# Optimization experiments

Measured on AMD Instinct MI355X. Metric: run time of the kernel, lower is better.

Reference implementation:

```python
import jax, jax.numpy as jnp
import numpy as np

TEMP = 0.07
EPS = 1e-6

B = 8192
D1 = 129  # d+1 ambient Lorentz coords


def setup_inputs() -> dict:
    key = jax.random.key(0)
    k1, k2 = jax.random.split(key)
    z1 = jax.random.normal(k1, (B, D1), dtype=jnp.float32)
    z2 = jax.random.normal(k2, (B, D1), dtype=jnp.float32)
    return {"z1": z1, "z2": z2}


def _loss(z1, z2):
    # Minkowski (Lorentz) inner product via a single GEMM:
    # <x,y>_L = -x0*y0 + sum_i xi*yi  ->  x @ (metric * y)^T
    metric = jnp.concatenate([-jnp.ones((1,), z1.dtype), jnp.ones((D1 - 1,), z1.dtype)])
    inner = jnp.einsum('bd,kd->bk', z1, z2 * metric)  # (B, B)
    # Lorentz distance with curvature c=1: acosh(clamp(-<x,y>_L, 1+eps))
    dist = jnp.arccosh(jnp.clip(-inner, 1.0 + EPS, None))
    sims = -dist / TEMP
    # symmetric InfoNCE: labels are the diagonal
    logp_t2i = jax.nn.log_softmax(sims, axis=-1)      # text -> image
    logp_i2t = jax.nn.log_softmax(sims.T, axis=-1)    # image -> text
    diag = jnp.arange(sims.shape[0])
    loss_t2i = -jnp.mean(logp_t2i[diag, diag])
    loss_i2t = -jnp.mean(logp_i2t[diag, diag])
    return (loss_t2i + loss_i2t) / 2.0


def reference(z1, z2):
    return _loss(z1, z2)
```

## Files before the change

### kernel.cpp

```cpp
#include <hip/hip_runtime.h>
#include <math.h>


#define BDIM   8192
#define K_IN   129
#define K_PAD  160
#define BK     32
#define NKT    (K_PAD / BK)
#define CTILES 8

typedef __bf16  bf16x8 __attribute__((ext_vector_type(8)));
typedef float   f32x4  __attribute__((ext_vector_type(4)));

#define OFF_A    0u
#define OFF_B    (BDIM * K_PAD * 2u)
#define OFF_RS   (2u * BDIM * K_PAD * 2u)
#define OFF_CP   (OFF_RS + BDIM * 4u)
#define OFF_DG   (OFF_CP + 4u * BDIM * 4u)

__device__ __forceinline__ float fast_sqrt(float x) {
#if __has_builtin(__builtin_amdgcn_sqrtf)
    return __builtin_amdgcn_sqrtf(x);
#else
    return sqrtf(x);
#endif
}
__device__ __forceinline__ float fast_log2(float x) {
#if __has_builtin(__builtin_amdgcn_logf)
    return __builtin_amdgcn_logf(x);
#else
    return __log2f(x);
#endif
}
__device__ __forceinline__ float fast_exp2(float x) {
#if __has_builtin(__builtin_amdgcn_exp2f)
    return __builtin_amdgcn_exp2f(x);
#else
    extern "C" __device__ float __ocml_native_exp2_f32(float);
    return __ocml_native_exp2_f32(x);
#endif
}

__device__ __forceinline__ unsigned short f2bf_rne(float f) {
    unsigned int u = __float_as_uint(f);
    u += 0x7FFFu + ((u >> 16) & 1u);
    return (unsigned short)(u >> 16);
}

__global__ __launch_bounds__(256) void convert_kernel(
    const float* __restrict__ z1, const float* __restrict__ z2,
    unsigned short* __restrict__ A, unsigned short* __restrict__ B,
    float* __restrict__ rs_cp)
{
    int idx = blockIdx.x * 256 + threadIdx.x;
    if (idx < 5 * BDIM) rs_cp[idx] = 0.f;
    if (idx >= BDIM * K_PAD) return;
    int r = idx / K_PAD;
    int c = idx - r * K_PAD;
    float va = 0.f, vb = 0.f;
    if (c < K_IN) {
        va = z1[r * K_IN + c];
        vb = z2[r * K_IN + c];
        if (c == 0) va = -va;
    }
    A[idx] = f2bf_rne(va);
    B[idx] = f2bf_rne(vb);
}


#define STAGE(bufidx, cb)                                                     \
    {                                                                         \
        const char* _gp = (const char*)(B + (size_t)(cb) * K_PAD)             \
                          + wave * 5120 + lane * 16;                          \
        unsigned short* _lp = &Bs[bufidx][wave * 2560];                       \
        _Pragma("unroll")                                                     \
        for (int _i = 0; _i < 5; ++_i)                                        \
            __builtin_amdgcn_global_load_lds(                                 \
                (const __attribute__((address_space(1))) void*)               \
                    (_gp + _i * 1024),                                        \
                (__attribute__((address_space(3))) void*)(_lp + _i * 512),    \
                16, 0, 0);                                                    \
    }

#define COMPUTE(bufidx, cb)                                                   \
    {                                                                         \
        const int colBase = (cb);                                             \
        const unsigned short* _Bt = &Bs[bufidx][0];                           \
        f32x4 acc[2][4] = {};                                                 \
        _Pragma("unroll")                                                     \
        for (int kt = 0; kt < NKT; ++kt) {                                    \
            bf16x8 bfr[4];                                                    \
            _Pragma("unroll")                                                 \
            for (int j = 0; j < 4; ++j)                                       \
                bfr[j] = *(const bf16x8*)                                     \
                    &_Bt[(l16 + j * 16) * K_PAD + quad * 8 + kt * BK];        \
            _Pragma("unroll")                                                 \
            for (int i = 0; i < 2; ++i)                                       \
                _Pragma("unroll")                                             \
                for (int j = 0; j < 4; ++j)                                   \
                    acc[i][j] = __builtin_amdgcn_mfma_f32_16x16x32_bf16(      \
                        Ah[i][kt], bfr[j], acc[i][j], 0, 0, 0);               \
        }                                                                     \
        const bool diagTile = (colBase == (rowBase & ~63));                   \
        const int  dj       = (rowBase >> 4) & 2;                             \
        float colp[4] = {0.f, 0.f, 0.f, 0.f};                                 \
        _Pragma("unroll")                                                     \
        for (int i = 0; i < 2; ++i) {                                         \
            _Pragma("unroll")                                                 \
            for (int j = 0; j < 4; ++j) {                                     \
                _Pragma("unroll")                                             \
                for (int reg = 0; reg < 4; ++reg) {                           \
                    float inner = acc[i][j][reg];                             \
                    float x = fmaxf(-inner, 1.000001f);                       \
                    float s = fast_sqrt(__builtin_fmaf(x, x, -1.0f));         \
                    float l2u = fast_log2(x + s);                             \
                    float e = fast_exp2(-14.285714285714286f * l2u);          \
                    rowp[i][reg] += e;                                        \
                    colp[j]      += e;                                        \
                    if (diagTile && (j - i) == dj && (quad * 4 + reg) == l16){\
                        int R = rowBase + i * 16 + quad * 4 + reg;            \
                        diag[R] = -9.902102579427789f * l2u;                  \
                    }                                                         \
                }                                                             \
            }                                                                 \
        }                                                                     \
        _Pragma("unroll")                                                     \
        for (int j = 0; j < 4; ++j) {                                         \
            float v = colp[j];                                                \
            v += __shfl_xor(v, 16);                                           \
            v += __shfl_xor(v, 32);                                           \
            if (quad == 0)                                                    \
                atomicAdd(&colRep[colBase + j * 16 + l16], v);                \
        }                                                                     \
    }

__global__ __launch_bounds__(256, 3) void gemm_epilogue_kernel(
    const unsigned short* __restrict__ A, const unsigned short* __restrict__ B,
    float* __restrict__ row_sum, float* __restrict__ col_part,
    float* __restrict__ diag)
{
    const int t    = threadIdx.x;
    const int lane = t & 63;
    const int wave = t >> 6;
    const int quad = lane >> 4;
    const int l16  = lane & 15;

    const int strip = blockIdx.x & 63;
    const int chunk = blockIdx.x >> 6;
    const int rowBase  = strip * 128 + wave * 32;
    const int colChunk = chunk * 512;

    const unsigned short* Abase = A + (rowBase + l16) * K_PAD + quad * 8;
    float* colRep = col_part + (strip & 3) * BDIM;

    __shared__ __align__(16) unsigned short Bs[2][64 * K_PAD];

    bf16x8 Ah[2][NKT];
    #pragma unroll
    for (int i = 0; i < 2; ++i)
        #pragma unroll
        for (int kt = 0; kt < NKT; ++kt)
            Ah[i][kt] = *(const bf16x8*)(Abase + i * 16 * K_PAD + kt * BK);

    float rowp[2][4] = {};

    STAGE(0, colChunk);
    __syncthreads();

    #pragma unroll 1
    for (int ct = 0; ct < CTILES; ++ct) {
        if (ct + 1 < CTILES)
            STAGE((ct + 1) & 1, colChunk + (ct + 1) * 64);
        COMPUTE(ct & 1, colChunk + ct * 64);
        __syncthreads();
    }

    #pragma unroll
    for (int i = 0; i < 2; ++i) {
        #pragma unroll
        for (int reg = 0; reg < 4; ++reg) {
            float v = rowp[i][reg];
            v += __shfl_xor(v, 1);
            v += __shfl_xor(v, 2);
            v += __shfl_xor(v, 4);
            v += __shfl_xor(v, 8);
            if (l16 == 0)
                atomicAdd(&row_sum[rowBase + i * 16 + quad * 4 + reg], v);
        }
    }
}

__global__ __launch_bounds__(1024) void finalize_kernel(
    const float* __restrict__ rs, const float* __restrict__ cp,
    const float* __restrict__ dg, float* __restrict__ out)
{
    __shared__ float part[16];
    int t = threadIdx.x;
    float a = 0.f;
    const float LN2_HALF = 0.34657359027997264f;
    for (int b = t; b < BDIM; b += 1024) {
        float cs = cp[b] + cp[b + BDIM] + cp[b + 2 * BDIM] + cp[b + 3 * BDIM];
        a += LN2_HALF * (fast_log2(rs[b]) + fast_log2(cs)) - dg[b];
    }
    #pragma unroll
    for (int m = 1; m < 64; m <<= 1) a += __shfl_xor(a, m);
    if ((t & 63) == 0) part[t >> 6] = a;
    __syncthreads();
    if (t < 16) {
        float v = part[t];
        #pragma unroll
        for (int m = 1; m < 16; m <<= 1) v += __shfl_xor(v, m);
        if (t == 0) out[0] = v * (1.0f / (float)BDIM);
    }
}

extern "C" void kernel_launch(void* const* d_in, const int* in_sizes, int n_in,
                              void* d_out, int out_size, void* d_ws, size_t ws_size,
                              hipStream_t stream)
{
    const float* z1 = (const float*)d_in[0];
    const float* z2 = (const float*)d_in[1];
    float* out = (float*)d_out;

    char* ws = (char*)d_ws;
    unsigned short* A  = (unsigned short*)(ws + OFF_A);
    unsigned short* B  = (unsigned short*)(ws + OFF_B);
    float* row_sum     = (float*)(ws + OFF_RS);
    float* col_part    = (float*)(ws + OFF_CP);
    float* diag        = (float*)(ws + OFF_DG);

    convert_kernel<<<(BDIM * K_PAD + 255) / 256, 256, 0, stream>>>(
        z1, z2, A, B, row_sum );

    gemm_epilogue_kernel<<<1024, 256, 0, stream>>>(
        A, B, row_sum, col_part, diag);

    finalize_kernel<<<1, 1024, 0, stream>>>(row_sum, col_part, diag, out);
}
```

Before: 108.8 us.

## Accumulate column sums in LDS and vectorize bf16 conversion stores

Column partial sums are now accumulated per block in a shared-memory array and flushed once to global memory with interleaved replica layout, instead of issuing global atomics every column tile. The convert kernel now writes 8 bf16 values per thread with vector stores, and the finalize kernel reads the four column replicas with one vector load. This reduces global atomic traffic and launch/thread count for conversion, at the cost of LDS atomics and a small extra shared buffer that may affect occupancy.

```diff
diff --git a/kernel.cpp b/kernel.cpp
--- a/kernel.cpp
+++ b/kernel.cpp
@@ -6,11 +6,12 @@
 #define K_IN   129
 #define K_PAD  160
 #define BK     32
-#define NKT    (K_PAD / BK)
+#define NKT    5
 #define CTILES 8
 
 typedef __bf16  bf16x8 __attribute__((ext_vector_type(8)));
 typedef float   f32x4  __attribute__((ext_vector_type(4)));
+typedef unsigned short u16x8 __attribute__((ext_vector_type(8)));
 
 #define OFF_A    0u
 #define OFF_B    (BDIM * K_PAD * 2u)
@@ -52,19 +53,26 @@
     unsigned short* __restrict__ A, unsigned short* __restrict__ B,
     float* __restrict__ rs_cp)
 {
-    int idx = blockIdx.x * 256 + threadIdx.x;
-    if (idx < 5 * BDIM) rs_cp[idx] = 0.f;
-    if (idx >= BDIM * K_PAD) return;
-    int r = idx / K_PAD;
-    int c = idx - r * K_PAD;
-    float va = 0.f, vb = 0.f;
-    if (c < K_IN) {
-        va = z1[r * K_IN + c];
-        vb = z2[r * K_IN + c];
-        if (c == 0) va = -va;
-    }
-    A[idx] = f2bf_rne(va);
-    B[idx] = f2bf_rne(vb);
+    int v = blockIdx.x * 256 + threadIdx.x;
+    if (v < 5 * BDIM) rs_cp[v] = 0.f;
+    if (v >= BDIM * (K_PAD / 8)) return;
+    int r  = v / (K_PAD / 8);
+    int c8 = (v - r * (K_PAD / 8)) * 8;
+    u16x8 a, b;
+    #pragma unroll
+    for (int i = 0; i < 8; ++i) {
+        int c = c8 + i;
+        float va = 0.f, vb = 0.f;
+        if (c < K_IN) {
+            va = z1[r * K_IN + c];
+            vb = z2[r * K_IN + c];
+            if (c == 0) va = -va;
+        }
+        a[i] = f2bf_rne(va);
+        b[i] = f2bf_rne(vb);
+    }
+    *(u16x8*)(A + r * K_PAD + c8) = a;
+    *(u16x8*)(B + r * K_PAD + c8) = b;
 }
 
 
@@ -130,7 +138,7 @@
             v += __shfl_xor(v, 16);                                           \
             v += __shfl_xor(v, 32);                                           \
             if (quad == 0)                                                    \
-                atomicAdd(&colRep[colBase + j * 16 + l16], v);                \
+                atomicAdd(&colAcc[(colBase - colChunk) + j * 16 + l16], v);   \
         }                                                                     \
     }
 
@@ -151,9 +159,11 @@
     const int colChunk = chunk * 512;
 
     const unsigned short* Abase = A + (rowBase + l16) * K_PAD + quad * 8;
-    float* colRep = col_part + (strip & 3) * BDIM;
 
     __shared__ __align__(16) unsigned short Bs[2][64 * K_PAD];
+    __shared__ float colAcc[512];
+
+    for (int c = t; c < 512; c += 256) colAcc[c] = 0.f;
 
     bf16x8 Ah[2][NKT];
     #pragma unroll
@@ -188,6 +198,9 @@
                 atomicAdd(&row_sum[rowBase + i * 16 + quad * 4 + reg], v);
         }
     }
+    const int rep = strip & 3;
+    for (int c = t; c < 512; c += 256)
+        atomicAdd(&col_part[(colChunk + c) * 4 + rep], colAcc[c]);
 }
 
 __global__ __launch_bounds__(1024) void finalize_kernel(
@@ -199,7 +212,8 @@
     float a = 0.f;
     const float LN2_HALF = 0.34657359027997264f;
     for (int b = t; b < BDIM; b += 1024) {
-        float cs = cp[b] + cp[b + BDIM] + cp[b + 2 * BDIM] + cp[b + 3 * BDIM];
+        f32x4 cv = *(const f32x4*)&cp[b * 4];
+        float cs = cv[0] + cv[1] + cv[2] + cv[3];
         a += LN2_HALF * (fast_log2(rs[b]) + fast_log2(cs)) - dg[b];
     }
     #pragma unroll
@@ -229,7 +243,7 @@
     float* col_part    = (float*)(ws + OFF_CP);
     float* diag        = (float*)(ws + OFF_DG);
 
-    convert_kernel<<<(BDIM * K_PAD + 255) / 256, 256, 0, stream>>>(
+    convert_kernel<<<(BDIM * (K_PAD / 8) + 255) / 256, 256, 0, stream>>>(
         z1, z2, A, B, row_sum );
 
     gemm_epilogue_kernel<<<1024, 256, 0, stream>>>(
```

New measurement: 118.5 us. +8.9%, slower.
